# Kernel tuning notes

Hardware: AMD Instinct MI355X
Metric: run time of the kernel (lower is better)

The kernel has to match this reference:

```python
import jax, jax.numpy as jnp
from jax import lax
import numpy as np

NUM_COEFF = 24      # solver.num_coeff_per_dim (Chebyshev coefficients)
NUM_POINTS = 48     # Chebyshev-Gauss collocation nodes per interval
PICARD_ITERS = 5    # fixed-point iterations of the spectral PAN solve


def _cheb_setup(dtype):
    j = jnp.arange(NUM_POINTS, dtype=dtype)
    n = jnp.arange(NUM_COEFF, dtype=dtype)
    # tau_j = cos(pi*(j+1/2)/P); T[n, j] = T_n(tau_j) = cos(n*arccos(tau_j))
    ang = jnp.pi * (j + 0.5) / NUM_POINTS
    T = jnp.cos(n[:, None] * ang[None, :])                  # [C, P]
    V = (2.0 / NUM_POINTS) * T
    V = V.at[0].mul(0.5)                                    # DCT: a_n = sum_j f(tau_j) V[n, j]
    signs = jnp.cos(n * jnp.pi)                             # T_n(-1) = (-1)^n
    return T, V, signs


def _cheb_antiderivative(a, signs):
    # Chebyshev coeffs of int_{-1}^{tau} f, given coeffs a of f: b_n = (a_{n-1}-a_{n+1})/(2n)
    C = a.shape[-1]
    a_pad = jnp.concatenate([a, jnp.zeros_like(a[..., :2])], axis=-1)
    n = jnp.arange(1, C, dtype=a.dtype)
    b_rest = (a_pad[..., 0:C - 1] - a_pad[..., 2:C + 1]) / (2.0 * n)
    b0 = -jnp.sum(b_rest * signs[1:], axis=-1, keepdims=True)  # enforce value 0 at tau=-1
    return jnp.concatenate([b0, b_rest], axis=-1)


def _vf(y, W1, b1, W2, b2):
    # neural vector field f(t, y): autonomous MLP
    return jnp.tanh(y @ W1 + b1) @ W2 + b2


def _pan_solve(y_init, t_span, W1, b1, W2, b2):
    # Chebyshev-spectral (PAN) ODE solve; returns trajectory at t_span points
    # and the per-interval coefficient tensors B_all [I, batch, dim, C]
    T, V, signs = _cheb_setup(y_init.dtype)

    def solve_interval(y0, ts):
        t0, t1 = ts[0], ts[1]
        scale = (t1 - t0) * 0.5                             # dtau -> dt Jacobian

        def picard(B, _):
            y_nodes = jnp.einsum('bdc,cp->pbd', B, T)       # y at collocation nodes
            fvals = _vf(y_nodes, W1, b1, W2, b2)            # [P, batch, dim]
            a = jnp.einsum('pbd,cp->bdc', fvals, V)         # Chebyshev coeffs of f
            Bn = scale * _cheb_antiderivative(a, signs)
            Bn = Bn.at[..., 0].add(y0)                      # y(tau=-1) = y0
            return Bn, None

        B0 = jnp.zeros((*y0.shape, NUM_COEFF), y0.dtype).at[..., 0].set(y0)
        B, _ = lax.scan(picard, B0, None, length=PICARD_ITERS)
        y1 = jnp.sum(B, axis=-1)                            # T_n(1) = 1
        return y1, (B, y1)

    ts = jnp.stack([t_span[:-1], t_span[1:]], axis=-1)      # [I, 2]
    _, (B_all, y_ends) = lax.scan(solve_interval, y_init, ts)
    traj = jnp.concatenate([y_init[None], y_ends], axis=0)  # [I+1, batch, dim]
    return traj, B_all


def setup_inputs() -> dict:
    key = jax.random.key(0)
    k1, k2, k3 = jax.random.split(key, 3)
    batch, dim, hidden = 256, 512, 512
    s = np.float32(1.0 / np.sqrt(dim))
    return {
        'y_init': jax.random.normal(k1, (batch, dim), jnp.float32),
        't_span': jnp.linspace(0.0, 1.0, 7, dtype=jnp.float32),
        'W1': s * jax.random.normal(k2, (dim, hidden), jnp.float32),
        'b1': jnp.zeros((hidden,), jnp.float32),
        'W2': s * jax.random.normal(k3, (hidden, dim), jnp.float32),
        'b2': jnp.zeros((dim,), jnp.float32),
    }


def reference(y_init, t_span, W1, b1, W2, b2):
    traj, _B_all = _pan_solve(y_init, t_span, W1, b1, W2, b2)
    return (t_span, traj)
```

## Files before the change

kernel.cpp:

```cpp
#include <hip/hip_runtime.h>
#include <hip/hip_bf16.h>
#include <math.h>

#define NC 24
#define NP 48
#define NI 6
#define BATCH 256
#define DIM 512
#define NELEM (BATCH*DIM)
#define PROWS (BATCH*NC)

typedef __bf16 bf16x8 __attribute__((ext_vector_type(8)));
typedef unsigned short u16x8 __attribute__((ext_vector_type(8)));
typedef float f32x4 __attribute__((ext_vector_type(4)));
using bf16 = __hip_bfloat16;

struct bq8 { __hip_bfloat162 a, b; };

__device__ __forceinline__ void gld_lds16(const void* g, void* l) {
  __builtin_amdgcn_global_load_lds(
      (const __attribute__((address_space(1))) void*)g,
      (__attribute__((address_space(3))) void*)l, 16, 0, 0);
}

__device__ __forceinline__ float fast_tanh(float x) {
  float u = __expf(2.0f * x);
  float r = __builtin_amdgcn_rcpf(u + 1.0f);
  return __builtin_fmaf(-2.0f, r, 1.0f);
}

__device__ __forceinline__ float bfu(unsigned short u) {
  union { unsigned int i; float f; } v; v.i = ((unsigned)u) << 16; return v.f;
}

__global__ void k_setup(const float* __restrict__ t_span, bf16* __restrict__ Tbf,
                        bf16* __restrict__ Abf, float* __restrict__ a1,
                        float* __restrict__ rs, float* __restrict__ wv,
                        float* __restrict__ scales, float* __restrict__ zbias,
                        float* __restrict__ out) {
  __shared__ double Tsh[NC][NP];
  __shared__ double Ashd[NC][NP];
  __shared__ double a1sh[NC];
  __shared__ double wsh[NP];
  int tid = threadIdx.x;
  for (int idx = tid; idx < NC*NP; idx += 64) {
    int c = idx / NP, p = idx % NP;
    Tsh[c][p] = cos((double)c * (M_PI * ((double)p + 0.5) / NP));
  }
  for (int idx = tid; idx < 32*64; idx += 64) Abf[idx] = __float2bfloat16(0.f);
  for (int idx = tid; idx < 48*32; idx += 64) Tbf[idx] = __float2bfloat16(0.f);
  __syncthreads();
  if (tid < NP) {
    int q = tid;
    double V[NC], K[NC];
    for (int c = 0; c < NC; c++) V[c] = (2.0/NP) * Tsh[c][q];
    V[0] *= 0.5;
    double s = 0.0;
    for (int n = 1; n < NC; n++) {
      double hi = (n+1 < NC) ? V[n+1] : 0.0;
      K[n] = (V[n-1] - hi) / (2.0*n);
      s += (n & 1) ? -K[n] : K[n];
    }
    K[0] = -s;
    double wsum = 0.0;
    for (int c = 0; c < NC; c++) wsum += K[c];
    wv[q] = (float)wsum;
    wsh[q] = wsum;
    for (int c = 0; c < NC; c++) {
      Ashd[c][q] = K[c];
      Abf[c*64 + q] = __float2bfloat16((float)K[c]);
    }
  }
  __syncthreads();
  if (tid < NC) {
    double s = 0.0;
    for (int q = 0; q < NP; q++) s += Ashd[tid][q];
    a1sh[tid] = s;
    a1[tid] = (float)s;
  }
  __syncthreads();
  if (tid < NP) {
    int p = tid;
    double r = 0.0;
    for (int c = 0; c < NC; c++) r += Tsh[c][p] * a1sh[c];
    rs[p] = (float)r;
    for (int c = 0; c < NC; c++) Tbf[p*32 + c] = __float2bfloat16((float)Tsh[c][p]);
  }
  if (tid == 0) {
    double s = 0.0;
    for (int q = 0; q < NP; q++) s += wsh[q];
    scales[6] = (float)s;
  }
  for (int idx = tid; idx < DIM; idx += 64) zbias[idx] = 0.f;
  if (tid < NI) scales[tid] = 0.5f*(t_span[tid+1]-t_span[tid]);
  if (tid < NI+1) out[tid] = t_span[tid];
}

__global__ void k_wt(const float* __restrict__ W1, const float* __restrict__ W2,
                     bf16* __restrict__ W1T, bf16* __restrict__ W2T,
                     bf16* __restrict__ W2bf) {
  int idx = blockIdx.x*256 + threadIdx.x;
  int k = idx >> 9, n = idx & 511;
  W1T[n*DIM + k] = __float2bfloat16(W1[idx]);
  W2T[n*DIM + k] = __float2bfloat16(W2[idx]);
  W2bf[idx]      = __float2bfloat16(W2[idx]);
}

__global__ void k_bb(const float* __restrict__ W1, const float* __restrict__ b2,
                     float* __restrict__ bb) {
  int h = blockIdx.x*256 + threadIdx.x;
  float s = 0.f;
  for (int d = 0; d < DIM; d++) s = fmaf(b2[d], W1[d*DIM + h], s);
  bb[h] = s;
}

__global__ void k_init(const float* __restrict__ y_init, float* __restrict__ y0,
                       bf16* __restrict__ y0bf, float* __restrict__ traj0) {
  int i = blockIdx.x*256 + threadIdx.x;
  float v = y_init[i];
  y0[i] = v; traj0[i] = v;
  y0bf[i] = __float2bfloat16(v);
}

template<int EPI>
__global__ __launch_bounds__(256, 3) void k_gemm(const bf16* __restrict__ A,
    const bf16* __restrict__ BT, const float* __restrict__ bias,
    bf16* __restrict__ outb, float* __restrict__ outf) {
  __shared__ bf16 sA[2][128*64];
  __shared__ bf16 sB[2][64*64];
  int tid = threadIdx.x;
  int lane = tid & 63, wid = tid >> 6;
  int q8 = gridDim.x >> 3;
  int tl = (blockIdx.x & 7)*q8 + (blockIdx.x >> 3);
  int bm = tl >> 3, bn = tl & 7;
  int row0 = bm*128, col0 = bn*64;
  int wr = wid >> 1, wc = wid & 1;
  int r16 = lane & 15, g = lane >> 4;

  f32x4 acc[4][2];
  #pragma unroll
  for (int m = 0; m < 4; m++)
    #pragma unroll
    for (int n = 0; n < 2; n++)
      acc[m][n] = {0.f, 0.f, 0.f, 0.f};

  auto stage = [&](int buf, int k0) {
    #pragma unroll
    for (int j = 0; j < 4; j++) {
      int cid = wid*64 + lane + j*256;
      int r = cid >> 3;
      int c = (cid & 7) ^ (r & 7);
      gld_lds16(A + (size_t)(row0 + r)*DIM + k0 + c*8,
                (char*)&sA[buf][0] + wid*1024 + j*4096);
    }
    #pragma unroll
    for (int j = 0; j < 2; j++) {
      int cid = wid*64 + lane + j*256;
      int r = cid >> 3;
      int c = (cid & 7) ^ (r & 7);
      gld_lds16(BT + (size_t)(col0 + r)*DIM + k0 + c*8,
                (char*)&sB[buf][0] + wid*1024 + j*4096);
    }
  };

  stage(0, 0);
  int cur = 0;
  for (int k0 = 0; k0 < DIM; k0 += 64) {
    if (k0 + 64 < DIM) {
      stage(cur ^ 1, k0 + 64);
      asm volatile("s_waitcnt vmcnt(6)" ::: "memory");
    } else {
      asm volatile("s_waitcnt vmcnt(0)" ::: "memory");
    }
    __builtin_amdgcn_s_barrier();
    #pragma unroll
    for (int kk = 0; kk < 2; kk++) {
      bf16x8 af[4], bfr[2];
      #pragma unroll
      for (int m = 0; m < 4; m++) {
        int r = wr*64 + m*16 + r16;
        af[m] = *(const bf16x8*)(&sA[cur][0] + r*64 + (((kk*4+g) ^ (r&7))*8));
      }
      #pragma unroll
      for (int n = 0; n < 2; n++) {
        int r = wc*32 + n*16 + r16;
        bfr[n] = *(const bf16x8*)(&sB[cur][0] + r*64 + (((kk*4+g) ^ (r&7))*8));
      }
      #pragma unroll
      for (int m = 0; m < 4; m++)
        #pragma unroll
        for (int n = 0; n < 2; n++)
          acc[m][n] = __builtin_amdgcn_mfma_f32_16x16x32_bf16(af[m], bfr[n], acc[m][n], 0, 0, 0);
    }
    __builtin_amdgcn_s_barrier();
    cur ^= 1;
  }

  #pragma unroll
  for (int m = 0; m < 4; m++) {
    int rowb = row0 + wr*64 + m*16 + g*4;
    #pragma unroll
    for (int n = 0; n < 2; n++) {
      int col = col0 + wc*32 + n*16 + r16;
      float bv = bias[col];
      #pragma unroll
      for (int r = 0; r < 4; r++) {
        float v = acc[m][n][r] + bv;
        size_t idx = (size_t)(rowb + r)*DIM + col;
        if constexpr (EPI == 1) {
          outb[idx] = __float2bfloat16(v);
        } else {
          outf[idx] = v;
          outb[idx] = __float2bfloat16(fast_tanh(v));
        }
      }
    }
  }
}

template<int MODE>
__global__ __launch_bounds__(256, 2) void k_iter(
    const bf16* __restrict__ Pin, const bf16* __restrict__ H1,
    const bf16* __restrict__ W21T, const float* __restrict__ Cg,
    const float* __restrict__ bbg, const bf16* __restrict__ Tbf,
    const bf16* __restrict__ Abf, const float* __restrict__ a1,
    const float* __restrict__ rsg, const float* __restrict__ wvg,
    const float* __restrict__ scales, int t, bf16* __restrict__ outp) {
  __shared__ char smem[49152];
  int tid = threadIdx.x;
  int lane = tid & 63, wid = tid >> 6;
  int r16 = lane & 15, g = lane >> 4;
  int q8 = gridDim.x >> 3;
  int tl = (blockIdx.x & 7)*q8 + (blockIdx.x >> 3);
  int bm = tl >> 2, bn = tl & 3;
  int col0 = bn*128;
  int bglob0 = bm*2;

  if constexpr (MODE != 0) {
    int row0 = bm*48;
    f32x4 acc[3][2];
    #pragma unroll
    for (int m = 0; m < 3; m++)
      #pragma unroll
      for (int n = 0; n < 2; n++)
        acc[m][n] = {0.f, 0.f, 0.f, 0.f};

    auto stage = [&](int buf, int k0) {
      #pragma unroll
      for (int j = 0; j < 2; j++) {
        if (lane < 48) {
          int cid = j*192 + wid*48 + lane;
          int r = cid >> 3, cc = (cid & 7) ^ (r & 7);
          gld_lds16(Pin + (size_t)(row0 + r)*DIM + k0 + cc*8,
                    smem + buf*6144 + j*3072 + wid*768);
        }
      }
      #pragma unroll
      for (int j = 0; j < 4; j++) {
        int cid = j*256 + wid*64 + lane;
        int r = cid >> 3, cc = (cid & 7) ^ (r & 7);
        gld_lds16(W21T + (size_t)(col0 + r)*DIM + k0 + cc*8,
                  smem + 12288 + buf*16384 + j*4096 + wid*1024);
      }
    };

    stage(0, 0);
    int cur = 0;
    for (int ks = 0; ks < 8; ks++) {
      if (ks < 7) {
        stage(cur ^ 1, (ks+1)*64);
        asm volatile("s_waitcnt vmcnt(6)" ::: "memory");
      } else {
        asm volatile("s_waitcnt vmcnt(0)" ::: "memory");
      }
      __builtin_amdgcn_s_barrier();
      const char* sAc = smem + cur*6144;
      const char* sBc = smem + 12288 + cur*16384;
      #pragma unroll
      for (int kk = 0; kk < 2; kk++) {
        bf16x8 af[3], bfr[2];
        #pragma unroll
        for (int m = 0; m < 3; m++) {
          int r = m*16 + r16;
          af[m] = *(const bf16x8*)(sAc + r*128 + ((kk*4+g) ^ (r&7))*16);
        }
        #pragma unroll
        for (int n = 0; n < 2; n++) {
          int r = wid*32 + n*16 + r16;
          bfr[n] = *(const bf16x8*)(sBc + r*128 + ((kk*4+g) ^ (r&7))*16);
        }
        #pragma unroll
        for (int m = 0; m < 3; m++)
          #pragma unroll
          for (int n = 0; n < 2; n++)
            acc[m][n] = __builtin_amdgcn_mfma_f32_16x16x32_bf16(af[m], bfr[n], acc[m][n], 0, 0, 0);
      }
      __builtin_amdgcn_s_barrier();
      cur ^= 1;
    }

    #pragma unroll
    for (int m = 0; m < 3; m++) {
      int rowf = m*16 + g*4;
      int b_loc = rowf >= 24 ? 1 : 0;
      int c0 = rowf - b_loc*24;
      int slot = c0 >> 3;
      int inb  = (c0*2) & 15;
      #pragma unroll
      for (int n = 0; n < 2; n++) {
        int h = wid*32 + n*16 + r16;
        char* ad = smem + b_loc*8192 + h*64 + (((slot ^ ((h>>1)&3)) << 4) | inb);
        bq8 v;
        v.a = __hip_bfloat162{__float2bfloat16(acc[m][n][0]), __float2bfloat16(acc[m][n][1])};
        v.b = __hip_bfloat162{__float2bfloat16(acc[m][n][2]), __float2bfloat16(acc[m][n][3])};
        *(bq8*)ad = v;
      }
    }
  } else {
    bf16* sH1 = (bf16*)(smem + 16384);
    #pragma unroll
    for (int j = 0; j < 4; j++) {
      int e = j*256 + tid;
      int b = e >> 9, k = e & 511;
      sH1[e] = H1[(size_t)(bglob0 + b)*DIM + k];
    }
    __syncthreads();
    int b = tid >> 7, hl = tid & 127;
    int hg = col0 + hl;
    const bf16* wrow = W21T + (size_t)hg*DIM;
    const bf16* hrow = sH1 + b*512;
    float g1 = 0.f;
    for (int ks = 0; ks < 64; ks++) {
      u16x8 w8 = *(const u16x8*)(wrow + ks*8);
      u16x8 h8 = *(const u16x8*)(hrow + ks*8);
      #pragma unroll
      for (int i = 0; i < 8; i++)
        g1 = fmaf(bfu(h8[i]), bfu(w8[i]), g1);
    }
    __syncthreads();
    int rot = ((hl>>1)&3) << 4;
    #pragma unroll
    for (int c = 0; c < NC; c++) {
      int lb = c*2;
      char* ad = smem + b*8192 + hl*64 + ((( (lb>>4) << 4) ^ rot) | (lb & 15));
      *(bf16*)ad = __float2bfloat16(a1[c]*g1);
    }
  }

  if (tid < 256) {
    int bz = tid >> 7, hz = tid & 127;
    *(f32x4*)(smem + bz*8192 + hz*64 + ((3 ^ ((hz>>1)&3)) << 4)) = f32x4{0.f,0.f,0.f,0.f};
  }
  __syncthreads();

  int b_w = wid >> 1;
  int h0 = (wid & 1) << 6;
  int bglob = bglob0 + b_w;
  float sc = scales[t];

  f32x4 acc2[3][4];
  #pragma unroll
  for (int pt = 0; pt < 3; pt++)
    #pragma unroll
    for (int n2 = 0; n2 < 4; n2++)
      acc2[pt][n2] = {0.f, 0.f, 0.f, 0.f};
  {
    bf16x8 afT[3];
    #pragma unroll
    for (int pt = 0; pt < 3; pt++)
      afT[pt] = *(const bf16x8*)(Tbf + (pt*16 + r16)*32 + g*8);
    #pragma unroll
    for (int n2 = 0; n2 < 4; n2++) {
      int h = h0 + n2*16 + r16;
      bf16x8 b8 = *(const bf16x8*)(smem + b_w*8192 + h*64 + ((g ^ ((h>>1)&3)) << 4));
      #pragma unroll
      for (int pt = 0; pt < 3; pt++)
        acc2[pt][n2] = __builtin_amdgcn_mfma_f32_16x16x32_bf16(afT[pt], b8, acc2[pt][n2], 0, 0, 0);
    }
  }

  float rsv[12];
  #pragma unroll
  for (int pt = 0; pt < 3; pt++)
    #pragma unroll
    for (int r = 0; r < 4; r++)
      rsv[pt*4+r] = rsg[pt*16 + g*4 + r];

  if constexpr (MODE == 2) {
    float wvv[12];
    #pragma unroll
    for (int pt = 0; pt < 3; pt++)
      #pragma unroll
      for (int r = 0; r < 4; r++)
        wvv[pt*4+r] = wvg[pt*16 + g*4 + r];
    #pragma unroll
    for (int n2 = 0; n2 < 4; n2++) {
      int hg2 = col0 + h0 + n2*16 + r16;
      float cv = Cg[(size_t)bglob*DIM + hg2];
      float bbv = bbg[hg2];
      float hw = 0.f;
      #pragma unroll
      for (int pt = 0; pt < 3; pt++)
        #pragma unroll
        for (int r = 0; r < 4; r++) {
          float z = fmaf(sc, fmaf(rsv[pt*4+r], bbv, acc2[pt][n2][r]), cv);
          hw = fmaf(wvv[pt*4+r], fast_tanh(z), hw);
        }
      hw += __shfl_xor(hw, 16);
      hw += __shfl_xor(hw, 32);
      if (g == 0)
        outp[(size_t)bglob*DIM + hg2] = __float2bfloat16(hw);
    }
    return;
  } else {
    #pragma unroll
    for (int n2 = 0; n2 < 4; n2++) {
      int h = h0 + n2*16 + r16;
      int hg2 = col0 + h;
      float cv = Cg[(size_t)bglob*DIM + hg2];
      float bbv = bbg[hg2];
      #pragma unroll
      for (int pt = 0; pt < 3; pt++) {
        int p0 = pt*16 + g*4;
        float th[4];
        #pragma unroll
        for (int r = 0; r < 4; r++) {
          float z = fmaf(sc, fmaf(rsv[pt*4+r], bbv, acc2[pt][n2][r]), cv);
          th[r] = fast_tanh(z);
        }
        char* ad = smem + 16384 + b_w*16384 + h*128 + ((p0*2) ^ ((h&7)<<4));
        bq8 v;
        v.a = __hip_bfloat162{__float2bfloat16(th[0]), __float2bfloat16(th[1])};
        v.b = __hip_bfloat162{__float2bfloat16(th[2]), __float2bfloat16(th[3])};
        *(bq8*)ad = v;
      }
    }
    if (tid < 256) {
      int bz = tid >> 7, hz = tid & 127;
      char* base = smem + 16384 + bz*16384 + hz*128;
      *(f32x4*)(base + (96  ^ ((hz&7)<<4))) = f32x4{0.f,0.f,0.f,0.f};
      *(f32x4*)(base + (112 ^ ((hz&7)<<4))) = f32x4{0.f,0.f,0.f,0.f};
    }
    __syncthreads();

    f32x4 acc3[2][4];
    #pragma unroll
    for (int ct = 0; ct < 2; ct++)
      #pragma unroll
      for (int n2 = 0; n2 < 4; n2++)
        acc3[ct][n2] = {0.f, 0.f, 0.f, 0.f};
    bf16x8 afA[2][2];
    #pragma unroll
    for (int ct = 0; ct < 2; ct++)
      #pragma unroll
      for (int kk = 0; kk < 2; kk++)
        afA[ct][kk] = *(const bf16x8*)(Abf + (ct*16 + r16)*64 + kk*32 + g*8);
    #pragma unroll
    for (int kk = 0; kk < 2; kk++) {
      #pragma unroll
      for (int n2 = 0; n2 < 4; n2++) {
        int h = h0 + n2*16 + r16;
        bf16x8 b8 = *(const bf16x8*)(smem + 16384 + b_w*16384 + h*128 +
                                     ((kk*64 + g*16) ^ ((h&7)<<4)));
        #pragma unroll
        for (int ct = 0; ct < 2; ct++)
          acc3[ct][n2] = __builtin_amdgcn_mfma_f32_16x16x32_bf16(afA[ct][kk], b8, acc3[ct][n2], 0, 0, 0);
      }
    }
    #pragma unroll
    for (int n2 = 0; n2 < 4; n2++) {
      int hg2 = col0 + h0 + n2*16 + r16;
      #pragma unroll
      for (int ct = 0; ct < 2; ct++) {
        if (ct == 1 && g >= 2) continue;
        #pragma unroll
        for (int r = 0; r < 4; r++) {
          int c = ct*16 + g*4 + r;
          outp[((size_t)(bglob*NC + c))*DIM + hg2] = __float2bfloat16(acc3[ct][n2][r]);
        }
      }
    }
  }
}

__global__ __launch_bounds__(256, 3) void k_next(const bf16* __restrict__ A,
    const bf16* __restrict__ W2T, const bf16* __restrict__ W21T,
    const float* __restrict__ b2, const float* __restrict__ bb,
    float* __restrict__ y0, bf16* __restrict__ y0bf, float* __restrict__ C,
    bf16* __restrict__ H1, const float* __restrict__ scales, int t,
    float* __restrict__ traj) {
  __shared__ bf16 sA[2][128*64];
  __shared__ bf16 sB[2][64*64];
  int tid = threadIdx.x;
  int lane = tid & 63, wid = tid >> 6;
  int q8 = gridDim.x >> 3;
  int tl = (blockIdx.x & 7)*q8 + (blockIdx.x >> 3);
  int bm = tl >> 4, bn = tl & 15;
  int half = bn >> 3;
  int row0 = bm*128, col0 = (bn & 7)*64;
  const bf16* BT = half ? W21T : W2T;
  int wr = wid >> 1, wc = wid & 1;
  int r16 = lane & 15, g = lane >> 4;

  f32x4 acc[4][2];
  #pragma unroll
  for (int m = 0; m < 4; m++)
    #pragma unroll
    for (int n = 0; n < 2; n++)
      acc[m][n] = {0.f, 0.f, 0.f, 0.f};

  auto stage = [&](int buf, int k0) {
    #pragma unroll
    for (int j = 0; j < 4; j++) {
      int cid = wid*64 + lane + j*256;
      int r = cid >> 3;
      int c = (cid & 7) ^ (r & 7);
      gld_lds16(A + (size_t)(row0 + r)*DIM + k0 + c*8,
                (char*)&sA[buf][0] + wid*1024 + j*4096);
    }
    #pragma unroll
    for (int j = 0; j < 2; j++) {
      int cid = wid*64 + lane + j*256;
      int r = cid >> 3;
      int c = (cid & 7) ^ (r & 7);
      gld_lds16(BT + (size_t)(col0 + r)*DIM + k0 + c*8,
                (char*)&sB[buf][0] + wid*1024 + j*4096);
    }
  };

  stage(0, 0);
  int cur = 0;
  for (int k0 = 0; k0 < DIM; k0 += 64) {
    if (k0 + 64 < DIM) {
      stage(cur ^ 1, k0 + 64);
      asm volatile("s_waitcnt vmcnt(6)" ::: "memory");
    } else {
      asm volatile("s_waitcnt vmcnt(0)" ::: "memory");
    }
    __builtin_amdgcn_s_barrier();
    #pragma unroll
    for (int kk = 0; kk < 2; kk++) {
      bf16x8 af[4], bfr[2];
      #pragma unroll
      for (int m = 0; m < 4; m++) {
        int r = wr*64 + m*16 + r16;
        af[m] = *(const bf16x8*)(&sA[cur][0] + r*64 + (((kk*4+g) ^ (r&7))*8));
      }
      #pragma unroll
      for (int n = 0; n < 2; n++) {
        int r = wc*32 + n*16 + r16;
        bfr[n] = *(const bf16x8*)(&sB[cur][0] + r*64 + (((kk*4+g) ^ (r&7))*8));
      }
      #pragma unroll
      for (int m = 0; m < 4; m++)
        #pragma unroll
        for (int n = 0; n < 2; n++)
          acc[m][n] = __builtin_amdgcn_mfma_f32_16x16x32_bf16(af[m], bfr[n], acc[m][n], 0, 0, 0);
    }
    __builtin_amdgcn_s_barrier();
    cur ^= 1;
  }

  float sc = scales[t];
  float sumw = scales[6];
  #pragma unroll
  for (int m = 0; m < 4; m++) {
    int rowb = row0 + wr*64 + m*16 + g*4;
    #pragma unroll
    for (int n = 0; n < 2; n++) {
      int col = col0 + wc*32 + n*16 + r16;
      #pragma unroll
      for (int r = 0; r < 4; r++) {
        size_t idx = (size_t)(rowb + r)*DIM + col;
        if (half == 0) {
          float bv = sumw * b2[col];
          float y1 = fmaf(sc, acc[m][n][r] + bv, y0[idx]);
          y0[idx] = y1;
          y0bf[idx] = __float2bfloat16(y1);
          traj[idx] = y1;
        } else {
          float cb = sc * sumw * bb[col];
          float cnew = fmaf(sc, acc[m][n][r], C[idx] + cb);
          C[idx] = cnew;
          H1[idx] = __float2bfloat16(fast_tanh(cnew));
        }
      }
    }
  }
}

extern "C" void kernel_launch(void* const* d_in, const int* in_sizes, int n_in,
                              void* d_out, int out_size, void* d_ws, size_t ws_size,
                              hipStream_t stream) {
  const float* y_init = (const float*)d_in[0];
  const float* t_span = (const float*)d_in[1];
  const float* W1 = (const float*)d_in[2];
  const float* b1 = (const float*)d_in[3];
  const float* W2 = (const float*)d_in[4];
  const float* b2 = (const float*)d_in[5];
  float* out = (float*)d_out;

  char* ws = (char*)d_ws;
  size_t off = 0;
  auto carve = [&](size_t bytes) {
    void* p = ws + off; off += (bytes + 255) & ~(size_t)255; return p;
  };
  bf16*  Tbf    = (bf16*) carve((size_t)48*32*2);
  bf16*  Abf    = (bf16*) carve((size_t)32*64*2);
  float* a1     = (float*)carve(NC*4);
  float* rs     = (float*)carve(NP*4);
  float* wv     = (float*)carve(NP*4);
  float* bb     = (float*)carve(DIM*4);
  float* scales = (float*)carve(8*4);
  float* zbias  = (float*)carve(DIM*4);
  float* y0     = (float*)carve((size_t)NELEM*4);
  float* C      = (float*)carve((size_t)NELEM*4);
  bf16*  y0bf   = (bf16*) carve((size_t)NELEM*2);
  bf16*  H1     = (bf16*) carve((size_t)NELEM*2);
  bf16*  Hw     = (bf16*) carve((size_t)NELEM*2);
  bf16*  W1T    = (bf16*) carve((size_t)DIM*DIM*2);
  bf16*  W2T    = (bf16*) carve((size_t)DIM*DIM*2);
  bf16*  W2bf   = (bf16*) carve((size_t)DIM*DIM*2);
  bf16*  W21T   = (bf16*) carve((size_t)DIM*DIM*2);
  bf16*  Pa     = (bf16*) carve((size_t)PROWS*DIM*2);
  bf16*  Pb     = (bf16*) carve((size_t)PROWS*DIM*2);

  k_setup<<<1, 64, 0, stream>>>(t_span, Tbf, Abf, a1, rs, wv, scales, zbias, out);
  k_wt<<<(DIM*DIM)/256, 256, 0, stream>>>(W1, W2, W1T, W2T, W2bf);
  k_bb<<<2, 256, 0, stream>>>(W1, b2, bb);
  k_gemm<1><<<32, 256, 0, stream>>>(W1T, W2bf, zbias, W21T, nullptr);
  k_init<<<NELEM/256, 256, 0, stream>>>(y_init, y0, y0bf, out + 7);
  k_gemm<2><<<16, 256, 0, stream>>>(y0bf, W1T, b1, H1, C);

  const int GRID = (BATCH/2)*(DIM/128);

  for (int t = 0; t < NI; t++) {
    k_iter<0><<<GRID, 256, 0, stream>>>(nullptr, H1, W21T, C, bb, Tbf, Abf,
                                        a1, rs, wv, scales, t, Pa);
    k_iter<1><<<GRID, 256, 0, stream>>>(Pa, nullptr, W21T, C, bb, Tbf, Abf,
                                        a1, rs, wv, scales, t, Pb);
    k_iter<1><<<GRID, 256, 0, stream>>>(Pb, nullptr, W21T, C, bb, Tbf, Abf,
                                        a1, rs, wv, scales, t, Pa);
    k_iter<2><<<GRID, 256, 0, stream>>>(Pa, nullptr, W21T, C, bb, Tbf, Abf,
                                        a1, rs, wv, scales, t, Hw);
    k_next<<<32, 256, 0, stream>>>(Hw, W2T, W21T, b2, bb, y0, y0bf, C, H1,
                                   scales, t, out + 7 + (size_t)(t+1)*NELEM);
  }
}
```

Before: 411.6 us.

## Double k_iter block to 4 batch rows with 512 threads sharing W21T tile

Each k_iter block now handles 4 batch elements (96 P-rows) instead of 2, using 8 waves in a 2x4 layout over the GEMM tile and halving the grid. The W21T tile staged into LDS is reused by twice as many rows, which cuts global/L2 traffic for the weight operand. The cost is 96KB dynamic LDS per block, which lowers occupancy and leaves fewer blocks (256) to fill the device. The wait count and staging offsets are adjusted to match.

```diff
diff --git a/kernel.cpp b/kernel.cpp
--- a/kernel.cpp
+++ b/kernel.cpp
@@ -219,14 +219,14 @@
 }
 
 template<int MODE>
-__global__ __launch_bounds__(256, 2) void k_iter(
+__global__ __launch_bounds__(512, 2) void k_iter(
     const bf16* __restrict__ Pin, const bf16* __restrict__ H1,
     const bf16* __restrict__ W21T, const float* __restrict__ Cg,
     const float* __restrict__ bbg, const bf16* __restrict__ Tbf,
     const bf16* __restrict__ Abf, const float* __restrict__ a1,
     const float* __restrict__ rsg, const float* __restrict__ wvg,
     const float* __restrict__ scales, int t, bf16* __restrict__ outp) {
-  __shared__ char smem[49152];
+  extern __shared__ char smem[];
   int tid = threadIdx.x;
   int lane = tid & 63, wid = tid >> 6;
   int r16 = lane & 15, g = lane >> 4;
@@ -234,10 +234,11 @@
   int tl = (blockIdx.x & 7)*q8 + (blockIdx.x >> 3);
   int bm = tl >> 2, bn = tl & 3;
   int col0 = bn*128;
-  int bglob0 = bm*2;
+  int bglob0 = bm*4;
 
   if constexpr (MODE != 0) {
-    int row0 = bm*48;
+    int row0 = bm*96;
+    int wr = wid >> 2, wc = wid & 3;
     f32x4 acc[3][2];
     #pragma unroll
     for (int m = 0; m < 3; m++)
@@ -246,21 +247,24 @@
         acc[m][n] = {0.f, 0.f, 0.f, 0.f};
 
     auto stage = [&](int buf, int k0) {
+      {
+        int cid = wid*64 + lane;
+        int r = cid >> 3, cc = (cid & 7) ^ (r & 7);
+        gld_lds16(Pin + (size_t)(row0 + r)*DIM + k0 + cc*8,
+                  smem + buf*12288 + wid*1024);
+      }
+      if (wid < 4) {
+        int cid = 512 + wid*64 + lane;
+        int r = cid >> 3, cc = (cid & 7) ^ (r & 7);
+        gld_lds16(Pin + (size_t)(row0 + r)*DIM + k0 + cc*8,
+                  smem + buf*12288 + 8192 + wid*1024);
+      }
       #pragma unroll
       for (int j = 0; j < 2; j++) {
-        if (lane < 48) {
-          int cid = j*192 + wid*48 + lane;
-          int r = cid >> 3, cc = (cid & 7) ^ (r & 7);
-          gld_lds16(Pin + (size_t)(row0 + r)*DIM + k0 + cc*8,
-                    smem + buf*6144 + j*3072 + wid*768);
-        }
-      }
-      #pragma unroll
-      for (int j = 0; j < 4; j++) {
-        int cid = j*256 + wid*64 + lane;
+        int cid = j*512 + wid*64 + lane;
         int r = cid >> 3, cc = (cid & 7) ^ (r & 7);
         gld_lds16(W21T + (size_t)(col0 + r)*DIM + k0 + cc*8,
-                  smem + 12288 + buf*16384 + j*4096 + wid*1024);
+                  smem + 24576 + buf*16384 + j*8192 + wid*1024);
       }
     };
 
@@ -269,24 +273,24 @@
     for (int ks = 0; ks < 8; ks++) {
       if (ks < 7) {
         stage(cur ^ 1, (ks+1)*64);
-        asm volatile("s_waitcnt vmcnt(6)" ::: "memory");
+        asm volatile("s_waitcnt vmcnt(3)" ::: "memory");
       } else {
         asm volatile("s_waitcnt vmcnt(0)" ::: "memory");
       }
       __builtin_amdgcn_s_barrier();
-      const char* sAc = smem + cur*6144;
-      const char* sBc = smem + 12288 + cur*16384;
+      const char* sAc = smem + cur*12288;
+      const char* sBc = smem + 24576 + cur*16384;
       #pragma unroll
       for (int kk = 0; kk < 2; kk++) {
         bf16x8 af[3], bfr[2];
         #pragma unroll
         for (int m = 0; m < 3; m++) {
-          int r = m*16 + r16;
+          int r = wr*48 + m*16 + r16;
           af[m] = *(const bf16x8*)(sAc + r*128 + ((kk*4+g) ^ (r&7))*16);
         }
         #pragma unroll
         for (int n = 0; n < 2; n++) {
-          int r = wid*32 + n*16 + r16;
+          int r = wc*32 + n*16 + r16;
           bfr[n] = *(const bf16x8*)(sBc + r*128 + ((kk*4+g) ^ (r&7))*16);
         }
         #pragma unroll
@@ -301,14 +305,14 @@
 
     #pragma unroll
     for (int m = 0; m < 3; m++) {
-      int rowf = m*16 + g*4;
-      int b_loc = rowf >= 24 ? 1 : 0;
+      int rowf = wr*48 + m*16 + g*4;
+      int b_loc = rowf / 24;
       int c0 = rowf - b_loc*24;
       int slot = c0 >> 3;
       int inb  = (c0*2) & 15;
       #pragma unroll
       for (int n = 0; n < 2; n++) {
-        int h = wid*32 + n*16 + r16;
+        int h = wc*32 + n*16 + r16;
         char* ad = smem + b_loc*8192 + h*64 + (((slot ^ ((h>>1)&3)) << 4) | inb);
         bq8 v;
         v.a = __hip_bfloat162{__float2bfloat16(acc[m][n][0]), __float2bfloat16(acc[m][n][1])};
@@ -317,10 +321,10 @@
       }
     }
   } else {
-    bf16* sH1 = (bf16*)(smem + 16384);
+    bf16* sH1 = (bf16*)(smem + 32768);
     #pragma unroll
     for (int j = 0; j < 4; j++) {
-      int e = j*256 + tid;
+      int e = j*512 + tid;
       int b = e >> 9, k = e & 511;
       sH1[e] = H1[(size_t)(bglob0 + b)*DIM + k];
     }
@@ -347,7 +351,7 @@
     }
   }
 
-  if (tid < 256) {
+  {
     int bz = tid >> 7, hz = tid & 127;
     *(f32x4*)(smem + bz*8192 + hz*64 + ((3 ^ ((hz>>1)&3)) << 4)) = f32x4{0.f,0.f,0.f,0.f};
   }
@@ -428,16 +432,16 @@
           float z = fmaf(sc, fmaf(rsv[pt*4+r], bbv, acc2[pt][n2][r]), cv);
           th[r] = fast_tanh(z);
         }
-        char* ad = smem + 16384 + b_w*16384 + h*128 + ((p0*2) ^ ((h&7)<<4));
+        char* ad = smem + 32768 + b_w*16384 + h*128 + ((p0*2) ^ ((h&7)<<4));
         bq8 v;
         v.a = __hip_bfloat162{__float2bfloat16(th[0]), __float2bfloat16(th[1])};
         v.b = __hip_bfloat162{__float2bfloat16(th[2]), __float2bfloat16(th[3])};
         *(bq8*)ad = v;
       }
     }
-    if (tid < 256) {
+    {
       int bz = tid >> 7, hz = tid & 127;
-      char* base = smem + 16384 + bz*16384 + hz*128;
+      char* base = smem + 32768 + bz*16384 + hz*128;
       *(f32x4*)(base + (96  ^ ((hz&7)<<4))) = f32x4{0.f,0.f,0.f,0.f};
       *(f32x4*)(base + (112 ^ ((hz&7)<<4))) = f32x4{0.f,0.f,0.f,0.f};
     }
@@ -460,7 +464,7 @@
       #pragma unroll
       for (int n2 = 0; n2 < 4; n2++) {
         int h = h0 + n2*16 + r16;
-        bf16x8 b8 = *(const bf16x8*)(smem + 16384 + b_w*16384 + h*128 +
+        bf16x8 b8 = *(const bf16x8*)(smem + 32768 + b_w*16384 + h*128 +
                                      ((kk*64 + g*16) ^ ((h&7)<<4)));
         #pragma unroll
         for (int ct = 0; ct < 2; ct++)
@@ -625,6 +629,14 @@
   bf16*  Pa     = (bf16*) carve((size_t)PROWS*DIM*2);
   bf16*  Pb     = (bf16*) carve((size_t)PROWS*DIM*2);
 
+  const int ITER_LDS = 98304;
+  hipFuncSetAttribute(reinterpret_cast<const void*>(&k_iter<0>),
+                      hipFuncAttributeMaxDynamicSharedMemorySize, ITER_LDS);
+  hipFuncSetAttribute(reinterpret_cast<const void*>(&k_iter<1>),
+                      hipFuncAttributeMaxDynamicSharedMemorySize, ITER_LDS);
+  hipFuncSetAttribute(reinterpret_cast<const void*>(&k_iter<2>),
+                      hipFuncAttributeMaxDynamicSharedMemorySize, ITER_LDS);
+
   k_setup<<<1, 64, 0, stream>>>(t_span, Tbf, Abf, a1, rs, wv, scales, zbias, out);
   k_wt<<<(DIM*DIM)/256, 256, 0, stream>>>(W1, W2, W1T, W2T, W2bf);
   k_bb<<<2, 256, 0, stream>>>(W1, b2, bb);
@@ -632,17 +644,17 @@
   k_init<<<NELEM/256, 256, 0, stream>>>(y_init, y0, y0bf, out + 7);
   k_gemm<2><<<16, 256, 0, stream>>>(y0bf, W1T, b1, H1, C);
 
-  const int GRID = (BATCH/2)*(DIM/128);
+  const int GRID = (BATCH/4)*(DIM/128);
 
   for (int t = 0; t < NI; t++) {
-    k_iter<0><<<GRID, 256, 0, stream>>>(nullptr, H1, W21T, C, bb, Tbf, Abf,
-                                        a1, rs, wv, scales, t, Pa);
-    k_iter<1><<<GRID, 256, 0, stream>>>(Pa, nullptr, W21T, C, bb, Tbf, Abf,
-                                        a1, rs, wv, scales, t, Pb);
-    k_iter<1><<<GRID, 256, 0, stream>>>(Pb, nullptr, W21T, C, bb, Tbf, Abf,
-                                        a1, rs, wv, scales, t, Pa);
-    k_iter<2><<<GRID, 256, 0, stream>>>(Pa, nullptr, W21T, C, bb, Tbf, Abf,
-                                        a1, rs, wv, scales, t, Hw);
+    k_iter<0><<<GRID, 512, ITER_LDS, stream>>>(nullptr, H1, W21T, C, bb, Tbf, Abf,
+                                               a1, rs, wv, scales, t, Pa);
+    k_iter<1><<<GRID, 512, ITER_LDS, stream>>>(Pa, nullptr, W21T, C, bb, Tbf, Abf,
+                                               a1, rs, wv, scales, t, Pb);
+    k_iter<1><<<GRID, 512, ITER_LDS, stream>>>(Pb, nullptr, W21T, C, bb, Tbf, Abf,
+                                               a1, rs, wv, scales, t, Pa);
+    k_iter<2><<<GRID, 512, ITER_LDS, stream>>>(Pa, nullptr, W21T, C, bb, Tbf, Abf,
+                                               a1, rs, wv, scales, t, Hw);
     k_next<<<32, 256, 0, stream>>>(Hw, W2T, W21T, b2, bb, y0, y0bf, C, H1,
                                    scales, t, out + 7 + (size_t)(t+1)*NELEM);
   }
```

After: 425.7 us. 1.03x slower.
